# Performance work log

Hardware: AMD Instinct MI355X
Metric: run time of the kernel (lower is better)

## Reference

```python
import jax, jax.numpy as jnp
import numpy as np

NUM_UNFOLDS = 6
TAU = 1.0
ELAPSED = 1.0

def setup_inputs() -> dict:
    key = jax.random.key(0)
    k1, k2, k3, k4 = jax.random.split(key, 4)
    B, D_IN, UNITS = 32768, 256, 512
    inputs = jax.random.normal(k1, (B, D_IN), dtype=jnp.float32)
    hidden_state = jax.random.normal(k2, (B, UNITS), dtype=jnp.float32)
    # glorot-ish scaling for kernel, orthogonal-ish (scaled normal) for recurrent
    kernel = jax.random.normal(k3, (D_IN, UNITS), dtype=jnp.float32) * (1.0 / np.sqrt(D_IN))
    recurrent_kernel = jax.random.normal(k4, (UNITS, UNITS), dtype=jnp.float32) * (1.0 / np.sqrt(UNITS))
    bias = jnp.zeros((UNITS,), dtype=jnp.float32)
    scale = jnp.ones((UNITS,), dtype=jnp.float32)
    return {"inputs": inputs, "hidden_state": hidden_state, "kernel": kernel,
            "recurrent_kernel": recurrent_kernel, "bias": bias, "scale": scale}

def _dfdt(x, h, kernel, recurrent_kernel, bias, scale):
    # dh = scale * tanh(x@K + h@R + b) - tau*h
    pre = x @ kernel + h @ recurrent_kernel + bias
    dh_in = scale * jnp.tanh(pre)
    return dh_in - h * TAU

def _rk4_step(x, h, dt, kernel, recurrent_kernel, bias, scale):
    k1 = _dfdt(x, h, kernel, recurrent_kernel, bias, scale)
    k2 = _dfdt(x, h + k1 * (dt * 0.5), kernel, recurrent_kernel, bias, scale)
    k3 = _dfdt(x, h + k2 * (dt * 0.5), kernel, recurrent_kernel, bias, scale)
    k4 = _dfdt(x, h + k3 * dt, kernel, recurrent_kernel, bias, scale)
    return h + dt * (k1 + 2.0 * k2 + 2.0 * k3 + k4) / 6.0

def reference(inputs, hidden_state, kernel, recurrent_kernel, bias, scale):
    dt = ELAPSED / NUM_UNFOLDS
    def body(h, _):
        return _rk4_step(inputs, h, dt, kernel, recurrent_kernel, bias, scale), None
    h, _ = jax.lax.scan(body, hidden_state, None, length=NUM_UNFOLDS)
    return h
```

## Files before the change

### kernel.cpp

```cpp
#include <hip/hip_runtime.h>

typedef unsigned int u32;
typedef unsigned short u16;
typedef __bf16 bf16x8 __attribute__((ext_vector_type(8)));
typedef float f32x16 __attribute__((ext_vector_type(16)));
typedef float f32x4v __attribute__((ext_vector_type(4)));
typedef u32 u32x4 __attribute__((ext_vector_type(4)));
typedef u32 u32x2 __attribute__((ext_vector_type(2)));

#define BATCH    32768
#define DIN      256
#define UNITS    512
#define BM       32
#define NTHREADS 512
#define NSTEP    6
#define DT       (1.0f/6.0f)
#define TANH_C   2.885390082f
#define SMEM_BYTES (32768 + 32768 + 16384)

__device__ __forceinline__ u16 f2bf(float f) {
  return __builtin_bit_cast(u16, (__bf16)f);
}
__device__ __forceinline__ float bf2f(u16 b) {
  return __builtin_bit_cast(float, (u32)b << 16);
}
__device__ __forceinline__ u32 pk2(float a, float b) {
  return (u32)f2bf(a) | ((u32)f2bf(b) << 16);
}
__device__ __forceinline__ float tanh_pre(float t) {
  float a = __builtin_amdgcn_exp2f(t);
  float r = __builtin_amdgcn_rcpf(a + 1.f);
  return __builtin_fmaf(-2.f, r, 1.f);
}

__global__ void pack_weights(const float* __restrict__ Km, const float* __restrict__ Rm,
                             u16* __restrict__ Kp, u16* __restrict__ Rp) {
  int c = blockIdx.x * 256 + threadIdx.x;
  if (c < 32768) {
    int n = c & 511, g = c >> 9;
    u32x4 p;
#pragma unroll
    for (int i = 0; i < 4; ++i) {
      u16 lo = f2bf(Rm[(g * 8 + 2 * i) * 512 + n] * TANH_C);
      u16 hh = f2bf(Rm[(g * 8 + 2 * i + 1) * 512 + n] * TANH_C);
      p[i] = (u32)lo | ((u32)hh << 16);
    }
    ((u32x4*)Rp)[c] = p;
  } else {
    int c2 = c - 32768;
    int n = c2 & 511, g = c2 >> 9;
    u32x4 p;
#pragma unroll
    for (int i = 0; i < 4; ++i) {
      u16 lo = f2bf(Km[(g * 8 + 2 * i) * 512 + n] * TANH_C);
      u16 hh = f2bf(Km[(g * 8 + 2 * i + 1) * 512 + n] * TANH_C);
      p[i] = (u32)lo | ((u32)hh << 16);
    }
    ((u32x4*)Kp)[c2] = p;
  }
}

__global__ __launch_bounds__(NTHREADS, 4)
void ctrnn_fused(const float* __restrict__ X, const float* __restrict__ H0,
                 const u16* __restrict__ Kp, const u16* __restrict__ Rp,
                 const float* __restrict__ bias, const float* __restrict__ scale,
                 float* __restrict__ out) {
  extern __shared__ char smem[];
  char* heA  = smem;
  float* h1L = (float*)(smem + 32768);
  u32* xkbL1 = (u32*)(smem + 65536);

  const int tid  = threadIdx.x;
  const int lane = tid & 63;
  const int wv   = tid >> 6;
  const int ln   = lane & 31, hi = lane >> 5;
  const long r0  = (long)blockIdx.x * BM;

  const int jc0  = wv * 64 + ln;
  const int jc1  = jc0 + 32;
  const int aoff = lane << 4;
  const int chunk0 = wv * 4 + (ln >> 4);
  const int cb0 = chunk0 * 1024 + (((ln >> 3) & 1) << 9) + ((ln & 7) << 1);
  const int U0  = ((hi << 2) ^ (chunk0 & 7)) << 4;
  const int U1  = U0 ^ 32;

  {
    const f32x4v* X4 = (const f32x4v*)(X + r0 * DIN);
#pragma unroll
    for (int i = 0; i < 4; ++i) {
      int flat = i * NTHREADS + tid;
      int m = flat >> 6, c4 = flat & 63;
      f32x4v v = X4[m * 64 + c4];
      u32x2 p;
      p.x = pk2(v.x, v.y);
      p.y = pk2(v.z, v.w);
      int chunk = c4 >> 2;
      int block = ((c4 >> 1) & 1) * 32 + (m & 31);
      int addr = chunk * 1024 + ((block ^ (chunk & 7)) << 4) + (c4 & 1) * 8;
      *(u32x2*)(heA + addr) = p;
    }
  }

  const float scl0 = scale[jc0], scl1 = scale[jc1];

  float h0[16];
#pragma unroll
  for (int r = 0; r < 16; ++r) {
    int m = (r & 3) + ((r >> 2) << 3) + hi * 4;
    h0[r] = H0[(r0 + m) * UNITS + jc0];
    h1L[r * NTHREADS + tid] = H0[(r0 + m) * UNITS + jc1];
  }

  __syncthreads();

  {
    f32x16 pre0, pre1;
    {
      float b0 = bias[jc0] * TANH_C, b1 = bias[jc1] * TANH_C;
#pragma unroll
      for (int r = 0; r < 16; ++r) { pre0[r] = b0; pre1[r] = b1; }
    }
    const u32x4* Kp4 = (const u32x4*)Kp;
#pragma unroll 2
    for (int kb = 0; kb < 16; ++kb) {
      bf16x8 a = __builtin_bit_cast(bf16x8,
          *(const u32x4*)(heA + kb * 1024 + (aoff ^ ((kb & 7) << 4))));
      bf16x8 b0 = __builtin_bit_cast(bf16x8, Kp4[(kb * 2 + hi) * 512 + jc0]);
      bf16x8 b1 = __builtin_bit_cast(bf16x8, Kp4[(kb * 2 + hi) * 512 + jc1]);
      pre0 = __builtin_amdgcn_mfma_f32_32x32x16_bf16(a, b0, pre0, 0, 0, 0);
      pre1 = __builtin_amdgcn_mfma_f32_32x32x16_bf16(a, b1, pre1, 0, 0, 0);
    }
    u32 xkbP0t[8];
#pragma unroll
    for (int i = 0; i < 8; ++i) {
      xkbP0t[i] = pk2(pre0[2 * i], pre0[2 * i + 1]);
      xkbL1[i * NTHREADS + tid] = pk2(pre1[2 * i], pre1[2 * i + 1]);
    }
    __syncthreads();

#pragma unroll
    for (int r = 0; r < 16; ++r) {
      int mm = (r & 3) + ((r >> 2) << 3);
      *(u16*)(heA + cb0 + ((mm << 4) ^ U0))        = f2bf(h0[r]);
      *(u16*)(heA + cb0 + 2048 + ((mm << 4) ^ U1)) = f2bf(h1L[r * NTHREADS + tid]);
    }
    __syncthreads();

    const u32x4* Rp4 = (const u32x4*)Rp;
    float acc0[16], acc1[16];
    u32 xkbP0[8];
#pragma unroll
    for (int i = 0; i < 8; ++i) xkbP0[i] = xkbP0t[i];

#pragma unroll 1
    for (int it = 0; it < NSTEP * 4; ++it) {
      const int ev = it & 3;
      const float wk = (ev == 1 || ev == 2) ? 2.f : 1.f;
      const float ce = (ev < 2) ? (DT * 0.5f) : DT;
      const bool ev0 = (ev == 0), ev3 = (ev == 3);
      const bool last = (it == NSTEP * 4 - 1);

      f32x16 p0, p1;
#pragma unroll
      for (int i = 0; i < 8; ++i) {
        u32 q0 = xkbP0[i];
        u32 q1 = xkbL1[i * NTHREADS + tid];
        p0[2 * i]     = bf2f((u16)(q0 & 0xffffu));
        p0[2 * i + 1] = bf2f((u16)(q0 >> 16));
        p1[2 * i]     = bf2f((u16)(q1 & 0xffffu));
        p1[2 * i + 1] = bf2f((u16)(q1 >> 16));
      }
#pragma unroll 2
      for (int kb = 0; kb < 32; ++kb) {
        bf16x8 a = __builtin_bit_cast(bf16x8,
            *(const u32x4*)(heA + kb * 1024 + (aoff ^ ((kb & 7) << 4))));
        bf16x8 b0 = __builtin_bit_cast(bf16x8, Rp4[(kb * 2 + hi) * 512 + jc0]);
        bf16x8 b1 = __builtin_bit_cast(bf16x8, Rp4[(kb * 2 + hi) * 512 + jc1]);
        p0 = __builtin_amdgcn_mfma_f32_32x32x16_bf16(a, b0, p0, 0, 0, 0);
        p1 = __builtin_amdgcn_mfma_f32_32x32x16_bf16(a, b1, p1, 0, 0, 0);
      }

#pragma unroll
      for (int r = 0; r < 16; ++r) {
        int mm = (r & 3) + ((r >> 2) << 3);
        float he = bf2f(*(const u16*)(heA + cb0 + ((mm << 4) ^ U0)));
        float k = __builtin_fmaf(scl0, tanh_pre(p0[r]), -he);
        acc0[r] = ev0 ? k : __builtin_fmaf(wk, k, acc0[r]);
        if (ev3) h0[r] += (DT / 6.f) * acc0[r];
        p0[r] = k;
      }
#pragma unroll
      for (int r = 0; r < 16; ++r) {
        int mm = (r & 3) + ((r >> 2) << 3);
        float he = bf2f(*(const u16*)(heA + cb0 + 2048 + ((mm << 4) ^ U1)));
        float k = __builtin_fmaf(scl1, tanh_pre(p1[r]), -he);
        acc1[r] = ev0 ? k : __builtin_fmaf(wk, k, acc1[r]);
        if (ev3) {
          float hv = h1L[r * NTHREADS + tid] + (DT / 6.f) * acc1[r];
          h1L[r * NTHREADS + tid] = hv;
        }
        p1[r] = k;
      }
      __syncthreads();

      if (!last) {
#pragma unroll
        for (int r = 0; r < 16; ++r) {
          int mm = (r & 3) + ((r >> 2) << 3);
          float v0 = ev3 ? h0[r] : __builtin_fmaf(ce, p0[r], h0[r]);
          *(u16*)(heA + cb0 + ((mm << 4) ^ U0)) = f2bf(v0);
          float hv = h1L[r * NTHREADS + tid];
          float v1 = ev3 ? hv : __builtin_fmaf(ce, p1[r], hv);
          *(u16*)(heA + cb0 + 2048 + ((mm << 4) ^ U1)) = f2bf(v1);
        }
        __syncthreads();
      }
    }
  }

#pragma unroll
  for (int r = 0; r < 16; ++r) {
    int m = (r & 3) + ((r >> 2) << 3) + hi * 4;
    out[(r0 + m) * UNITS + jc0] = h0[r];
    out[(r0 + m) * UNITS + jc1] = h1L[r * NTHREADS + tid];
  }
}

extern "C" void kernel_launch(void* const* d_in, const int* in_sizes, int n_in,
                              void* d_out, int out_size, void* d_ws, size_t ws_size,
                              hipStream_t stream) {
  const float* X     = (const float*)d_in[0];
  const float* H0    = (const float*)d_in[1];
  const float* Km    = (const float*)d_in[2];
  const float* Rm    = (const float*)d_in[3];
  const float* bias  = (const float*)d_in[4];
  const float* scale = (const float*)d_in[5];
  float* out = (float*)d_out;

  u16* Rp = (u16*)d_ws;
  u16* Kp = Rp + UNITS * UNITS;

  (void)hipFuncSetAttribute((const void*)ctrnn_fused,
                            hipFuncAttributeMaxDynamicSharedMemorySize, SMEM_BYTES);

  pack_weights<<<192, 256, 0, stream>>>(Km, Rm, Kp, Rp);
  ctrnn_fused<<<BATCH / BM, NTHREADS, SMEM_BYTES, stream>>>(X, H0, Kp, Rp, bias, scale, out);
}
```

Baseline: 625.5 us.

## Double-buffer stage activations in LDS and move h1/xkb state to registers

```diff
diff --git a/kernel.cpp b/kernel.cpp
--- a/kernel.cpp
+++ b/kernel.cpp
@@ -16,7 +16,7 @@
 #define NSTEP    6
 #define DT       (1.0f/6.0f)
 #define TANH_C   2.885390082f
-#define SMEM_BYTES (32768 + 32768 + 16384)
+#define SMEM_BYTES (2 * 32768)
 
 __device__ __forceinline__ u16 f2bf(float f) {
   return __builtin_bit_cast(u16, (__bf16)f);
@@ -66,9 +66,7 @@
                  const float* __restrict__ bias, const float* __restrict__ scale,
                  float* __restrict__ out) {
   extern __shared__ char smem[];
-  char* heA  = smem;
-  float* h1L = (float*)(smem + 32768);
-  u32* xkbL1 = (u32*)(smem + 65536);
+  char* heA = smem;
 
   const int tid  = threadIdx.x;
   const int lane = tid & 63;
@@ -103,16 +101,17 @@
 
   const float scl0 = scale[jc0], scl1 = scale[jc1];
 
-  float h0[16];
+  float h0[16], h1[16];
 #pragma unroll
   for (int r = 0; r < 16; ++r) {
     int m = (r & 3) + ((r >> 2) << 3) + hi * 4;
     h0[r] = H0[(r0 + m) * UNITS + jc0];
-    h1L[r * NTHREADS + tid] = H0[(r0 + m) * UNITS + jc1];
+    h1[r] = H0[(r0 + m) * UNITS + jc1];
   }
 
   __syncthreads();
 
+  u32 xkbP0[8], xkbP1[8];
   {
     f32x16 pre0, pre1;
     {
@@ -130,99 +129,85 @@
       pre0 = __builtin_amdgcn_mfma_f32_32x32x16_bf16(a, b0, pre0, 0, 0, 0);
       pre1 = __builtin_amdgcn_mfma_f32_32x32x16_bf16(a, b1, pre1, 0, 0, 0);
     }
-    u32 xkbP0t[8];
 #pragma unroll
     for (int i = 0; i < 8; ++i) {
-      xkbP0t[i] = pk2(pre0[2 * i], pre0[2 * i + 1]);
-      xkbL1[i * NTHREADS + tid] = pk2(pre1[2 * i], pre1[2 * i + 1]);
-    }
-    __syncthreads();
+      xkbP0[i] = pk2(pre0[2 * i], pre0[2 * i + 1]);
+      xkbP1[i] = pk2(pre1[2 * i], pre1[2 * i + 1]);
+    }
+  }
+  __syncthreads();
+
+#pragma unroll
+  for (int r = 0; r < 16; ++r) {
+    int mm = (r & 3) + ((r >> 2) << 3);
+    *(u16*)(heA + cb0 + ((mm << 4) ^ U0))        = f2bf(h0[r]);
+    *(u16*)(heA + cb0 + 2048 + ((mm << 4) ^ U1)) = f2bf(h1[r]);
+  }
+  __syncthreads();
+
+  const u32x4* Rp4 = (const u32x4*)Rp;
+  float acc0[16], acc1[16];
+  int p = 0;
+
+#pragma unroll 1
+  for (int it = 0; it < NSTEP * 4; ++it) {
+    const int ev = it & 3;
+    const float wk = (ev == 1 || ev == 2) ? 2.f : 1.f;
+    const float ce = (ev < 2) ? (DT * 0.5f) : DT;
+    const bool ev0 = (ev == 0), ev3 = (ev == 3);
+    const bool last = (it == NSTEP * 4 - 1);
+    const char* bufR = heA + p * 32768;
+    char* bufW = heA + (p ^ 1) * 32768;
+
+    f32x16 p0, p1;
+#pragma unroll
+    for (int i = 0; i < 8; ++i) {
+      u32 q0 = xkbP0[i];
+      u32 q1 = xkbP1[i];
+      p0[2 * i]     = bf2f((u16)(q0 & 0xffffu));
+      p0[2 * i + 1] = bf2f((u16)(q0 >> 16));
+      p1[2 * i]     = bf2f((u16)(q1 & 0xffffu));
+      p1[2 * i + 1] = bf2f((u16)(q1 >> 16));
+    }
+#pragma unroll 2
+    for (int kb = 0; kb < 32; ++kb) {
+      bf16x8 a = __builtin_bit_cast(bf16x8,
+          *(const u32x4*)(bufR + kb * 1024 + (aoff ^ ((kb & 7) << 4))));
+      bf16x8 b0 = __builtin_bit_cast(bf16x8, Rp4[(kb * 2 + hi) * 512 + jc0]);
+      bf16x8 b1 = __builtin_bit_cast(bf16x8, Rp4[(kb * 2 + hi) * 512 + jc1]);
+      p0 = __builtin_amdgcn_mfma_f32_32x32x16_bf16(a, b0, p0, 0, 0, 0);
+      p1 = __builtin_amdgcn_mfma_f32_32x32x16_bf16(a, b1, p1, 0, 0, 0);
+    }
 
 #pragma unroll
     for (int r = 0; r < 16; ++r) {
       int mm = (r & 3) + ((r >> 2) << 3);
-      *(u16*)(heA + cb0 + ((mm << 4) ^ U0))        = f2bf(h0[r]);
-      *(u16*)(heA + cb0 + 2048 + ((mm << 4) ^ U1)) = f2bf(h1L[r * NTHREADS + tid]);
-    }
-    __syncthreads();
-
-    const u32x4* Rp4 = (const u32x4*)Rp;
-    float acc0[16], acc1[16];
-    u32 xkbP0[8];
-#pragma unroll
-    for (int i = 0; i < 8; ++i) xkbP0[i] = xkbP0t[i];
-
-#pragma unroll 1
-    for (int it = 0; it < NSTEP * 4; ++it) {
-      const int ev = it & 3;
-      const float wk = (ev == 1 || ev == 2) ? 2.f : 1.f;
-      const float ce = (ev < 2) ? (DT * 0.5f) : DT;
-      const bool ev0 = (ev == 0), ev3 = (ev == 3);
-      const bool last = (it == NSTEP * 4 - 1);
-
-      f32x16 p0, p1;
-#pragma unroll
-      for (int i = 0; i < 8; ++i) {
-        u32 q0 = xkbP0[i];
-        u32 q1 = xkbL1[i * NTHREADS + tid];
-        p0[2 * i]     = bf2f((u16)(q0 & 0xffffu));
-        p0[2 * i + 1] = bf2f((u16)(q0 >> 16));
-        p1[2 * i]     = bf2f((u16)(q1 & 0xffffu));
-        p1[2 * i + 1] = bf2f((u16)(q1 >> 16));
+      float he0 = bf2f(*(const u16*)(bufR + cb0 + ((mm << 4) ^ U0)));
+      float he1 = bf2f(*(const u16*)(bufR + cb0 + 2048 + ((mm << 4) ^ U1)));
+      float k0 = __builtin_fmaf(scl0, tanh_pre(p0[r]), -he0);
+      float k1 = __builtin_fmaf(scl1, tanh_pre(p1[r]), -he1);
+      acc0[r] = ev0 ? k0 : __builtin_fmaf(wk, k0, acc0[r]);
+      acc1[r] = ev0 ? k1 : __builtin_fmaf(wk, k1, acc1[r]);
+      if (ev3) {
+        h0[r] += (DT / 6.f) * acc0[r];
+        h1[r] += (DT / 6.f) * acc1[r];
       }
-#pragma unroll 2
-      for (int kb = 0; kb < 32; ++kb) {
-        bf16x8 a = __builtin_bit_cast(bf16x8,
-            *(const u32x4*)(heA + kb * 1024 + (aoff ^ ((kb & 7) << 4))));
-        bf16x8 b0 = __builtin_bit_cast(bf16x8, Rp4[(kb * 2 + hi) * 512 + jc0]);
-        bf16x8 b1 = __builtin_bit_cast(bf16x8, Rp4[(kb * 2 + hi) * 512 + jc1]);
-        p0 = __builtin_amdgcn_mfma_f32_32x32x16_bf16(a, b0, p0, 0, 0, 0);
-        p1 = __builtin_amdgcn_mfma_f32_32x32x16_bf16(a, b1, p1, 0, 0, 0);
+      if (!last) {
+        float v0 = ev3 ? h0[r] : __builtin_fmaf(ce, k0, h0[r]);
+        float v1 = ev3 ? h1[r] : __builtin_fmaf(ce, k1, h1[r]);
+        *(u16*)(bufW + cb0 + ((mm << 4) ^ U0))        = f2bf(v0);
+        *(u16*)(bufW + cb0 + 2048 + ((mm << 4) ^ U1)) = f2bf(v1);
       }
-
-#pragma unroll
-      for (int r = 0; r < 16; ++r) {
-        int mm = (r & 3) + ((r >> 2) << 3);
-        float he = bf2f(*(const u16*)(heA + cb0 + ((mm << 4) ^ U0)));
-        float k = __builtin_fmaf(scl0, tanh_pre(p0[r]), -he);
-        acc0[r] = ev0 ? k : __builtin_fmaf(wk, k, acc0[r]);
-        if (ev3) h0[r] += (DT / 6.f) * acc0[r];
-        p0[r] = k;
-      }
-#pragma unroll
-      for (int r = 0; r < 16; ++r) {
-        int mm = (r & 3) + ((r >> 2) << 3);
-        float he = bf2f(*(const u16*)(heA + cb0 + 2048 + ((mm << 4) ^ U1)));
-        float k = __builtin_fmaf(scl1, tanh_pre(p1[r]), -he);
-        acc1[r] = ev0 ? k : __builtin_fmaf(wk, k, acc1[r]);
-        if (ev3) {
-          float hv = h1L[r * NTHREADS + tid] + (DT / 6.f) * acc1[r];
-          h1L[r * NTHREADS + tid] = hv;
-        }
-        p1[r] = k;
-      }
-      __syncthreads();
-
-      if (!last) {
-#pragma unroll
-        for (int r = 0; r < 16; ++r) {
-          int mm = (r & 3) + ((r >> 2) << 3);
-          float v0 = ev3 ? h0[r] : __builtin_fmaf(ce, p0[r], h0[r]);
-          *(u16*)(heA + cb0 + ((mm << 4) ^ U0)) = f2bf(v0);
-          float hv = h1L[r * NTHREADS + tid];
-          float v1 = ev3 ? hv : __builtin_fmaf(ce, p1[r], hv);
-          *(u16*)(heA + cb0 + 2048 + ((mm << 4) ^ U1)) = f2bf(v1);
-        }
-        __syncthreads();
-      }
-    }
+    }
+    if (!last) __syncthreads();
+    p ^= 1;
   }
 
 #pragma unroll
   for (int r = 0; r < 16; ++r) {
     int m = (r & 3) + ((r >> 2) << 3) + hi * 4;
     out[(r0 + m) * UNITS + jc0] = h0[r];
-    out[(r0 + m) * UNITS + jc1] = h1L[r * NTHREADS + tid];
+    out[(r0 + m) * UNITS + jc1] = h1[r];
   }
 }
 
```

After: 701.4 us. +12.1%, slower.
